# Performance work log

Hardware: AMD Instinct MI355X
Metric: run time of the kernel (lower is better)

The kernel has to match this reference:

```python
import jax, jax.numpy as jnp
import numpy as np

NEG_INF = -1.0e9  # matches torch masked_fill value (unused: no mask)

def setup_inputs() -> dict:
    key = jax.random.key(0)
    kq, kk, kv = jax.random.split(key, 3)
    B, Sq, Sk, D = 8, 2048, 2048, 512
    return {
        "query": jax.random.normal(kq, (B, Sq, D), dtype=jnp.float32),
        "key": jax.random.normal(kk, (B, Sk, D), dtype=jnp.float32),
        "value": jax.random.normal(kv, (B, Sk, D), dtype=jnp.float32),
        "temperature": jnp.ones((), dtype=jnp.float32),
    }

def reference(query, key, value, temperature):
    # Squared Euclidean distance via GEMM identity: ||q||^2 + ||k||^2 - 2 q.k
    # (same math as the broadcast sum((q-k)^2, -1), but without [B,Sq,Sk,D] tensor)
    q_sq = jnp.sum(query * query, axis=-1, keepdims=True)          # [B,Sq,1]
    k_sq = jnp.sum(key * key, axis=-1)[:, None, :]                 # [B,1,Sk]
    qk = jnp.einsum("bqd,bkd->bqk", query, key)                    # [B,Sq,Sk]
    distance_squared = q_sq + k_sq - 2.0 * qk
    similarity = -distance_squared / temperature
    attention_weights = jax.nn.softmax(similarity, axis=-1)        # [B,Sq,Sk]
    attended_values = jnp.einsum("bqk,bkd->bqd", attention_weights, value)
    return attended_values, attention_weights
```

## Files before the change

kernel.cpp:

```cpp
#include <hip/hip_runtime.h>

typedef __bf16 bf16_t;
typedef __bf16 bf16x8 __attribute__((ext_vector_type(8)));
typedef __bf16 bf16x4 __attribute__((ext_vector_type(4)));
typedef __bf16 bf16x2 __attribute__((ext_vector_type(2)));
typedef float f32x4 __attribute__((ext_vector_type(4)));

#define NB 8
#define SQ 2048
#define SK 2048
#define DD 512

#define BM 128
#define BN 128
#define BK 32
#define LDK 40
#define NBLK (SK / BN)

__global__ __launch_bounds__(256, 2) void logits_kernel(
    const float* __restrict__ Q, const float* __restrict__ K,
    const float* __restrict__ tempP, float* __restrict__ logits,
    float* __restrict__ Mpart, float* __restrict__ Spart) {
  __shared__ bf16_t qh[BM][LDK], ql[BM][LDK], kh[BN][LDK], kl[BN][LDK];
  __shared__ float ksred[BN][8];
  __shared__ float mred[BM][2], sred[BM][2];
  const int b = blockIdx.z;
  const int m0 = blockIdx.y * BM;
  const int n0 = blockIdx.x * BN;
  const int tid = threadIdx.x;
  const int lane = tid & 63;
  const int wave = tid >> 6;
  const int wm = (wave >> 1) * 64;
  const int wn = (wave & 1) * 64;
  const int lrow = lane & 15;
  const int quad = lane >> 4;

  const float* Qb = Q + (size_t)b * SQ * DD;
  const float* Kb = K + (size_t)b * SK * DD;

  const int srow = tid >> 3;
  const int scol = (tid & 7) * 4;

  const float* qbase = Qb + (size_t)(m0 + srow) * DD + scol;
  const float* kbase = Kb + (size_t)(n0 + srow) * DD + scol;

  f32x4 acc[4][4];
#pragma unroll
  for (int i = 0; i < 4; i++)
#pragma unroll
    for (int j = 0; j < 4; j++) acc[i][j] = (f32x4){0.f, 0.f, 0.f, 0.f};

  float kss[4] = {0.f, 0.f, 0.f, 0.f};

  float4 pq[4], pk[4];
#pragma unroll
  for (int i = 0; i < 4; i++) {
    pq[i] = *(const float4*)(qbase + (size_t)i * 32 * DD);
    pk[i] = *(const float4*)(kbase + (size_t)i * 32 * DD);
  }

  for (int k0 = 0; k0 < DD; k0 += BK) {
    __syncthreads();
#pragma unroll
    for (int i = 0; i < 4; i++) {
      const int r = srow + i * 32;
      float4 qv = pq[i], kv = pk[i];
      bf16_t q0 = (bf16_t)qv.x, q1 = (bf16_t)qv.y, q2 = (bf16_t)qv.z, q3 = (bf16_t)qv.w;
      bf16x4 qhv = {q0, q1, q2, q3};
      bf16x4 qlv = {(bf16_t)(qv.x - (float)q0), (bf16_t)(qv.y - (float)q1),
                    (bf16_t)(qv.z - (float)q2), (bf16_t)(qv.w - (float)q3)};
      bf16_t c0 = (bf16_t)kv.x, c1 = (bf16_t)kv.y, c2 = (bf16_t)kv.z, c3 = (bf16_t)kv.w;
      bf16x4 khv = {c0, c1, c2, c3};
      bf16x4 klv = {(bf16_t)(kv.x - (float)c0), (bf16_t)(kv.y - (float)c1),
                    (bf16_t)(kv.z - (float)c2), (bf16_t)(kv.w - (float)c3)};
      *(bf16x4*)&qh[r][scol] = qhv;
      *(bf16x4*)&ql[r][scol] = qlv;
      *(bf16x4*)&kh[r][scol] = khv;
      *(bf16x4*)&kl[r][scol] = klv;
      kss[i] = fmaf(kv.x, kv.x, kss[i]);
      kss[i] = fmaf(kv.y, kv.y, kss[i]);
      kss[i] = fmaf(kv.z, kv.z, kss[i]);
      kss[i] = fmaf(kv.w, kv.w, kss[i]);
    }
    __syncthreads();

    if (k0 + BK < DD) {
#pragma unroll
      for (int i = 0; i < 4; i++) {
        pq[i] = *(const float4*)(qbase + (size_t)i * 32 * DD + (k0 + BK));
        pk[i] = *(const float4*)(kbase + (size_t)i * 32 * DD + (k0 + BK));
      }
    }

    bf16x8 bh[4], bl[4];
#pragma unroll
    for (int ni = 0; ni < 4; ni++) {
      bh[ni] = *(const bf16x8*)&kh[wn + ni * 16 + lrow][quad * 8];
      bl[ni] = *(const bf16x8*)&kl[wn + ni * 16 + lrow][quad * 8];
    }
#pragma unroll
    for (int mi = 0; mi < 4; mi++) {
      bf16x8 ah = *(const bf16x8*)&qh[wm + mi * 16 + lrow][quad * 8];
      bf16x8 al = *(const bf16x8*)&ql[wm + mi * 16 + lrow][quad * 8];
#pragma unroll
      for (int ni = 0; ni < 4; ni++) {
        acc[mi][ni] = __builtin_amdgcn_mfma_f32_16x16x32_bf16(ah, bh[ni], acc[mi][ni], 0, 0, 0);
        acc[mi][ni] = __builtin_amdgcn_mfma_f32_16x16x32_bf16(ah, bl[ni], acc[mi][ni], 0, 0, 0);
        acc[mi][ni] = __builtin_amdgcn_mfma_f32_16x16x32_bf16(al, bh[ni], acc[mi][ni], 0, 0, 0);
      }
    }
  }

#pragma unroll
  for (int i = 0; i < 4; i++) ksred[srow + i * 32][tid & 7] = kss[i];
  __syncthreads();

  const float invT = 1.0f / tempP[0];
  float* Lb = logits + (size_t)b * SQ * SK;
  float ks4[4];
#pragma unroll
  for (int ni = 0; ni < 4; ni++) {
    const float* kr = ksred[wn + ni * 16 + lrow];
    ks4[ni] = ((kr[0] + kr[1]) + (kr[2] + kr[3])) +
              ((kr[4] + kr[5]) + (kr[6] + kr[7]));
  }

#pragma unroll
  for (int mi = 0; mi < 4; mi++) {
#pragma unroll
    for (int r = 0; r < 4; r++) {
      const int row = wm + mi * 16 + quad * 4 + r;
      float sv[4];
#pragma unroll
      for (int ni = 0; ni < 4; ni++) {
        sv[ni] = (2.0f * acc[mi][ni][r] - ks4[ni]) * invT;
        Lb[(size_t)(m0 + row) * SK + (n0 + wn + ni * 16 + lrow)] = sv[ni];
      }
      float rm = fmaxf(fmaxf(sv[0], sv[1]), fmaxf(sv[2], sv[3]));
      rm = fmaxf(rm, __shfl_xor(rm, 1));
      rm = fmaxf(rm, __shfl_xor(rm, 2));
      rm = fmaxf(rm, __shfl_xor(rm, 4));
      rm = fmaxf(rm, __shfl_xor(rm, 8));
      float rs = __expf(sv[0] - rm) + __expf(sv[1] - rm) +
                 __expf(sv[2] - rm) + __expf(sv[3] - rm);
      rs += __shfl_xor(rs, 1);
      rs += __shfl_xor(rs, 2);
      rs += __shfl_xor(rs, 4);
      rs += __shfl_xor(rs, 8);
      if (lrow == 0) {
        mred[row][wave & 1] = rm;
        sred[row][wave & 1] = rs;
      }
    }
  }
  __syncthreads();
  if (tid < BM) {
    const float ma = mred[tid][0], mb = mred[tid][1];
    const float M = fmaxf(ma, mb);
    const float S = sred[tid][0] * __expf(ma - M) + sred[tid][1] * __expf(mb - M);
    const size_t o = ((size_t)b * NBLK + blockIdx.x) * SQ + (m0 + tid);
    Mpart[o] = M;
    Spart[o] = S;
  }
}

__global__ __launch_bounds__(256) void vt_kernel(const float* __restrict__ V,
                                                 bf16_t* __restrict__ Vt) {
  const int b = blockIdx.y;
  const int k0 = blockIdx.x * 32;
  const int tid = threadIdx.x;
  const int p = tid & 15;
  const int c = tid >> 4;
  const float* Vb = V + (size_t)b * SK * DD;
  bf16_t* Vtb = Vt + (size_t)b * DD * SK;
  const int k = k0 + 2 * p;
#pragma unroll
  for (int j = 0; j < 8; j++) {
    const int d0 = 4 * c + 64 * j;
    float4 v0 = *(const float4*)(Vb + (size_t)k * DD + d0);
    float4 v1 = *(const float4*)(Vb + (size_t)(k + 1) * DD + d0);
    bf16x2 t0 = {(bf16_t)v0.x, (bf16_t)v1.x};
    bf16x2 t1 = {(bf16_t)v0.y, (bf16_t)v1.y};
    bf16x2 t2 = {(bf16_t)v0.z, (bf16_t)v1.z};
    bf16x2 t3 = {(bf16_t)v0.w, (bf16_t)v1.w};
    *(bf16x2*)(Vtb + (size_t)(d0 + 0) * SK + k) = t0;
    *(bf16x2*)(Vtb + (size_t)(d0 + 1) * SK + k) = t1;
    *(bf16x2*)(Vtb + (size_t)(d0 + 2) * SK + k) = t2;
    *(bf16x2*)(Vtb + (size_t)(d0 + 3) * SK + k) = t3;
  }
}

#define PM 64

__global__ __launch_bounds__(512, 2) void pv_kernel(
    float* __restrict__ L,
    const bf16_t* __restrict__ Vt,
    const float* __restrict__ Mpart, const float* __restrict__ Spart,
    float* __restrict__ O) {
  __shared__ float Msh[PM], Ssh[PM];
  const int bid = blockIdx.x;
  const int b = bid & 7;
  const int m0 = (bid >> 3) * PM;
  const int tid = threadIdx.x;
  const int lane = tid & 63;
  const int wave = tid >> 6;
  const int wn = wave * 64;
  const int lrow = lane & 15;
  const int quad = lane >> 4;

  float* Lb = L + (size_t)b * SQ * SK;
  const bf16_t* Vtb = Vt + (size_t)b * DD * SK;

  if (tid < 4 * PM) {
    const int row = tid >> 2;
    const int i0 = (tid & 3) * 4;
    float pm[4], ps[4];
#pragma unroll
    for (int j = 0; j < 4; j++) {
      const size_t o = ((size_t)b * NBLK + (i0 + j)) * SQ + (m0 + row);
      pm[j] = Mpart[o];
      ps[j] = Spart[o];
    }
    float m = fmaxf(fmaxf(pm[0], pm[1]), fmaxf(pm[2], pm[3]));
    m = fmaxf(m, __shfl_xor(m, 1));
    m = fmaxf(m, __shfl_xor(m, 2));
    float s = ps[0] * __expf(pm[0] - m) + ps[1] * __expf(pm[1] - m) +
              ps[2] * __expf(pm[2] - m) + ps[3] * __expf(pm[3] - m);
    s += __shfl_xor(s, 1);
    s += __shfl_xor(s, 2);
    if ((tid & 3) == 0) {
      Msh[row] = m;
      Ssh[row] = 1.0f / s;
    }
  }
  __syncthreads();

  float Mv[4], Sv[4];
  float* Arow[4];
  const bf16_t* Brow[4];
#pragma unroll
  for (int i = 0; i < 4; i++) {
    const int r = i * 16 + lrow;
    Mv[i] = Msh[r];
    Sv[i] = Ssh[r];
    Arow[i] = Lb + (size_t)(m0 + r) * SK + quad * 8;
    Brow[i] = Vtb + (size_t)(wn + r) * SK + quad * 8;
  }

  f32x4 acc[4][4];
#pragma unroll
  for (int i = 0; i < 4; i++)
#pragma unroll
    for (int j = 0; j < 4; j++) acc[i][j] = (f32x4){0.f, 0.f, 0.f, 0.f};

  float4 rawA[4][2], rawB[4][2];
  bf16x8 bb[4];

#pragma unroll
  for (int mi = 0; mi < 4; mi++) {
    rawA[mi][0] = *(const float4*)(Arow[mi]);
    rawA[mi][1] = *(const float4*)(Arow[mi] + 4);
    rawB[mi][0] = *(const float4*)(Arow[mi] + BK);
    rawB[mi][1] = *(const float4*)(Arow[mi] + BK + 4);
  }
#pragma unroll
  for (int ni = 0; ni < 4; ni++) bb[ni] = *(const bf16x8*)(Brow[ni]);

  auto process = [&](float4 (&buf)[4][2], const int kw) {
    float4 nw[4][2];
    bf16x8 af[4];
#pragma unroll
    for (int mi = 0; mi < 4; mi++) {
      float4 r0 = buf[mi][0], r1 = buf[mi][1];
      float e0 = __expf(r0.x - Mv[mi]) * Sv[mi];
      float e1 = __expf(r0.y - Mv[mi]) * Sv[mi];
      float e2 = __expf(r0.z - Mv[mi]) * Sv[mi];
      float e3 = __expf(r0.w - Mv[mi]) * Sv[mi];
      float e4 = __expf(r1.x - Mv[mi]) * Sv[mi];
      float e5 = __expf(r1.y - Mv[mi]) * Sv[mi];
      float e6 = __expf(r1.z - Mv[mi]) * Sv[mi];
      float e7 = __expf(r1.w - Mv[mi]) * Sv[mi];
      nw[mi][0] = make_float4(e0, e1, e2, e3);
      nw[mi][1] = make_float4(e4, e5, e6, e7);
      af[mi] = (bf16x8){(bf16_t)e0, (bf16_t)e1, (bf16_t)e2, (bf16_t)e3,
                        (bf16_t)e4, (bf16_t)e5, (bf16_t)e6, (bf16_t)e7};
    }
    if (kw + 2 * BK < SK) {
#pragma unroll
      for (int mi = 0; mi < 4; mi++) {
        buf[mi][0] = *(const float4*)(Arow[mi] + kw + 2 * BK);
        buf[mi][1] = *(const float4*)(Arow[mi] + kw + 2 * BK + 4);
      }
    }
#pragma unroll
    for (int mi = 0; mi < 4; mi++)
#pragma unroll
      for (int ni = 0; ni < 4; ni++)
        acc[mi][ni] = __builtin_amdgcn_mfma_f32_16x16x32_bf16(af[mi], bb[ni],
                                                              acc[mi][ni], 0, 0, 0);
    if (kw + BK < SK) {
#pragma unroll
      for (int ni = 0; ni < 4; ni++)
        bb[ni] = *(const bf16x8*)(Brow[ni] + kw + BK);
    }
    asm volatile("s_barrier" ::: "memory");
    if (wave == 0) {
#pragma unroll
      for (int mi = 0; mi < 4; mi++) {
        *(float4*)(Arow[mi] + kw) = nw[mi][0];
        *(float4*)(Arow[mi] + kw + 4) = nw[mi][1];
      }
    }
  };

  for (int k0 = 0; k0 < SK; k0 += 2 * BK) {
    process(rawA, k0);
    process(rawB, k0 + BK);
  }

  float* Ob = O + (size_t)b * SQ * DD;
#pragma unroll
  for (int ni = 0; ni < 4; ni++) {
    const int d = wn + ni * 16 + lrow;
#pragma unroll
    for (int mi = 0; mi < 4; mi++) {
      const int mbase = m0 + mi * 16 + quad * 4;
#pragma unroll
      for (int r = 0; r < 4; r++) {
        Ob[(size_t)(mbase + r) * DD + d] = acc[mi][ni][r];
      }
    }
  }
}

extern "C" void kernel_launch(void* const* d_in, const int* in_sizes, int n_in,
                              void* d_out, int out_size, void* d_ws, size_t ws_size,
                              hipStream_t stream) {
  const float* Q = (const float*)d_in[0];
  const float* K = (const float*)d_in[1];
  const float* V = (const float*)d_in[2];
  const float* T = (const float*)d_in[3];

  float* outv = (float*)d_out;
  float* logits = outv + (size_t)NB * SQ * DD;

  float* Mpart = (float*)d_ws;
  float* Spart = Mpart + (size_t)NB * NBLK * SQ;
  bf16_t* Vt = (bf16_t*)(Spart + (size_t)NB * NBLK * SQ);

  vt_kernel<<<dim3(SK / 32, NB), 256, 0, stream>>>(V, Vt);
  logits_kernel<<<dim3(SK / BN, SQ / BM, NB), 256, 0, stream>>>(Q, K, T, logits,
                                                                Mpart, Spart);
  pv_kernel<<<dim3(NB * (SQ / PM)), 512, 0, stream>>>(logits, Vt, Mpart, Spart, outv);
}
```

Measured before the change: 509.0 us.

## Stage normalized softmax rows in swizzled LDS before the PV MFMA loop

```diff
diff --git a/kernel.cpp b/kernel.cpp
--- a/kernel.cpp
+++ b/kernel.cpp
@@ -190,132 +190,124 @@
   }
 }
 
-#define PM 64
-
-__global__ __launch_bounds__(512, 2) void pv_kernel(
+#define PM 32
+
+__device__ __forceinline__ unsigned lds_addr(int row, unsigned kb) {
+  return (unsigned)row * 4096u + (kb ^ (unsigned)((row & 7) << 4));
+}
+
+__global__ __launch_bounds__(512, 1) void pv_kernel(
     float* __restrict__ L,
     const bf16_t* __restrict__ Vt,
     const float* __restrict__ Mpart, const float* __restrict__ Spart,
     float* __restrict__ O) {
+  __shared__ __align__(16) unsigned char wlds[PM * 4096];
   __shared__ float Msh[PM], Ssh[PM];
   const int bid = blockIdx.x;
   const int b = bid & 7;
   const int m0 = (bid >> 3) * PM;
   const int tid = threadIdx.x;
+
+  float* Lb = L + (size_t)b * SQ * SK;
+  const bf16_t* Vtb = Vt + (size_t)b * DD * SK;
+
+  {
+    const int row = tid >> 4;
+    const int j = tid & 15;
+    const size_t o = ((size_t)b * NBLK + j) * SQ + (m0 + row);
+    const float pm = Mpart[o];
+    const float ps = Spart[o];
+    float m = pm;
+    m = fmaxf(m, __shfl_xor(m, 1));
+    m = fmaxf(m, __shfl_xor(m, 2));
+    m = fmaxf(m, __shfl_xor(m, 4));
+    m = fmaxf(m, __shfl_xor(m, 8));
+    float s = ps * __expf(pm - m);
+    s += __shfl_xor(s, 1);
+    s += __shfl_xor(s, 2);
+    s += __shfl_xor(s, 4);
+    s += __shfl_xor(s, 8);
+    if (j == 0) {
+      Msh[row] = m;
+      Ssh[row] = 1.0f / s;
+    }
+  }
+  __syncthreads();
+
+  {
+    const int row = tid >> 4;
+    const int g = tid & 15;
+    float* lp = Lb + (size_t)(m0 + row) * SK;
+    const float M = Msh[row];
+    const float invS = Ssh[row];
+#pragma unroll 8
+    for (int j = 0; j < 32; j++) {
+      const int k = g * 4 + j * 64;
+      float4 v = *(const float4*)(lp + k);
+      const float w0 = __expf(v.x - M) * invS;
+      const float w1 = __expf(v.y - M) * invS;
+      const float w2 = __expf(v.z - M) * invS;
+      const float w3 = __expf(v.w - M) * invS;
+      *(float4*)(lp + k) = make_float4(w0, w1, w2, w3);
+      bf16x4 w4 = {(bf16_t)w0, (bf16_t)w1, (bf16_t)w2, (bf16_t)w3};
+      *(bf16x4*)(wlds + lds_addr(row, (unsigned)(k * 2))) = w4;
+    }
+  }
+  __syncthreads();
+
   const int lane = tid & 63;
   const int wave = tid >> 6;
   const int wn = wave * 64;
   const int lrow = lane & 15;
   const int quad = lane >> 4;
 
-  float* Lb = L + (size_t)b * SQ * SK;
-  const bf16_t* Vtb = Vt + (size_t)b * DD * SK;
-
-  if (tid < 4 * PM) {
-    const int row = tid >> 2;
-    const int i0 = (tid & 3) * 4;
-    float pm[4], ps[4];
-#pragma unroll
-    for (int j = 0; j < 4; j++) {
-      const size_t o = ((size_t)b * NBLK + (i0 + j)) * SQ + (m0 + row);
-      pm[j] = Mpart[o];
-      ps[j] = Spart[o];
-    }
-    float m = fmaxf(fmaxf(pm[0], pm[1]), fmaxf(pm[2], pm[3]));
-    m = fmaxf(m, __shfl_xor(m, 1));
-    m = fmaxf(m, __shfl_xor(m, 2));
-    float s = ps[0] * __expf(pm[0] - m) + ps[1] * __expf(pm[1] - m) +
-              ps[2] * __expf(pm[2] - m) + ps[3] * __expf(pm[3] - m);
-    s += __shfl_xor(s, 1);
-    s += __shfl_xor(s, 2);
-    if ((tid & 3) == 0) {
-      Msh[row] = m;
-      Ssh[row] = 1.0f / s;
-    }
-  }
-  __syncthreads();
-
-  float Mv[4], Sv[4];
-  float* Arow[4];
   const bf16_t* Brow[4];
 #pragma unroll
-  for (int i = 0; i < 4; i++) {
-    const int r = i * 16 + lrow;
-    Mv[i] = Msh[r];
-    Sv[i] = Ssh[r];
-    Arow[i] = Lb + (size_t)(m0 + r) * SK + quad * 8;
-    Brow[i] = Vtb + (size_t)(wn + r) * SK + quad * 8;
-  }
-
-  f32x4 acc[4][4];
-#pragma unroll
-  for (int i = 0; i < 4; i++)
+  for (int ni = 0; ni < 4; ni++)
+    Brow[ni] = Vtb + (size_t)(wn + ni * 16 + lrow) * SK + quad * 8;
+
+  f32x4 acc[2][4];
+#pragma unroll
+  for (int i = 0; i < 2; i++)
 #pragma unroll
     for (int j = 0; j < 4; j++) acc[i][j] = (f32x4){0.f, 0.f, 0.f, 0.f};
 
-  float4 rawA[4][2], rawB[4][2];
-  bf16x8 bb[4];
-
-#pragma unroll
-  for (int mi = 0; mi < 4; mi++) {
-    rawA[mi][0] = *(const float4*)(Arow[mi]);
-    rawA[mi][1] = *(const float4*)(Arow[mi] + 4);
-    rawB[mi][0] = *(const float4*)(Arow[mi] + BK);
-    rawB[mi][1] = *(const float4*)(Arow[mi] + BK + 4);
-  }
-#pragma unroll
-  for (int ni = 0; ni < 4; ni++) bb[ni] = *(const bf16x8*)(Brow[ni]);
-
-  auto process = [&](float4 (&buf)[4][2], const int kw) {
-    float4 nw[4][2];
-    bf16x8 af[4];
-#pragma unroll
-    for (int mi = 0; mi < 4; mi++) {
-      float4 r0 = buf[mi][0], r1 = buf[mi][1];
-      float e0 = __expf(r0.x - Mv[mi]) * Sv[mi];
-      float e1 = __expf(r0.y - Mv[mi]) * Sv[mi];
-      float e2 = __expf(r0.z - Mv[mi]) * Sv[mi];
-      float e3 = __expf(r0.w - Mv[mi]) * Sv[mi];
-      float e4 = __expf(r1.x - Mv[mi]) * Sv[mi];
-      float e5 = __expf(r1.y - Mv[mi]) * Sv[mi];
-      float e6 = __expf(r1.z - Mv[mi]) * Sv[mi];
-      float e7 = __expf(r1.w - Mv[mi]) * Sv[mi];
-      nw[mi][0] = make_float4(e0, e1, e2, e3);
-      nw[mi][1] = make_float4(e4, e5, e6, e7);
-      af[mi] = (bf16x8){(bf16_t)e0, (bf16_t)e1, (bf16_t)e2, (bf16_t)e3,
-                        (bf16_t)e4, (bf16_t)e5, (bf16_t)e6, (bf16_t)e7};
-    }
-    if (kw + 2 * BK < SK) {
-#pragma unroll
-      for (int mi = 0; mi < 4; mi++) {
-        buf[mi][0] = *(const float4*)(Arow[mi] + kw + 2 * BK);
-        buf[mi][1] = *(const float4*)(Arow[mi] + kw + 2 * BK + 4);
-      }
-    }
-#pragma unroll
-    for (int mi = 0; mi < 4; mi++)
+  bf16x8 b0[4], b1[4];
+#pragma unroll
+  for (int ni = 0; ni < 4; ni++) b0[ni] = *(const bf16x8*)(Brow[ni]);
+#pragma unroll
+  for (int ni = 0; ni < 4; ni++) b1[ni] = *(const bf16x8*)(Brow[ni] + BK);
+
+  for (int k0 = 0; k0 < SK; k0 += 2 * BK) {
+    bf16x8 a0[2], a1[2];
+#pragma unroll
+    for (int mi = 0; mi < 2; mi++) {
+      const int row = mi * 16 + lrow;
+      a0[mi] = *(const bf16x8*)(wlds + lds_addr(row, (unsigned)((k0 + quad * 8) * 2)));
+      a1[mi] = *(const bf16x8*)(wlds + lds_addr(row, (unsigned)((k0 + BK + quad * 8) * 2)));
+    }
+#pragma unroll
+    for (int mi = 0; mi < 2; mi++)
 #pragma unroll
       for (int ni = 0; ni < 4; ni++)
-        acc[mi][ni] = __builtin_amdgcn_mfma_f32_16x16x32_bf16(af[mi], bb[ni],
+        acc[mi][ni] = __builtin_amdgcn_mfma_f32_16x16x32_bf16(a0[mi], b0[ni],
                                                               acc[mi][ni], 0, 0, 0);
-    if (kw + BK < SK) {
+    if (k0 + 2 * BK < SK) {
 #pragma unroll
       for (int ni = 0; ni < 4; ni++)
-        bb[ni] = *(const bf16x8*)(Brow[ni] + kw + BK);
-    }
-    asm volatile("s_barrier" ::: "memory");
-    if (wave == 0) {
-#pragma unroll
-      for (int mi = 0; mi < 4; mi++) {
-        *(float4*)(Arow[mi] + kw) = nw[mi][0];
-        *(float4*)(Arow[mi] + kw + 4) = nw[mi][1];
-      }
-    }
-  };
-
-  for (int k0 = 0; k0 < SK; k0 += 2 * BK) {
-    process(rawA, k0);
-    process(rawB, k0 + BK);
+        b0[ni] = *(const bf16x8*)(Brow[ni] + k0 + 2 * BK);
+    }
+#pragma unroll
+    for (int mi = 0; mi < 2; mi++)
+#pragma unroll
+      for (int ni = 0; ni < 4; ni++)
+        acc[mi][ni] = __builtin_amdgcn_mfma_f32_16x16x32_bf16(a1[mi], b1[ni],
+                                                              acc[mi][ni], 0, 0, 0);
+    if (k0 + 3 * BK < SK) {
+#pragma unroll
+      for (int ni = 0; ni < 4; ni++)
+        b1[ni] = *(const bf16x8*)(Brow[ni] + k0 + 3 * BK);
+    }
   }
 
   float* Ob = O + (size_t)b * SQ * DD;
@@ -323,7 +315,7 @@
   for (int ni = 0; ni < 4; ni++) {
     const int d = wn + ni * 16 + lrow;
 #pragma unroll
-    for (int mi = 0; mi < 4; mi++) {
+    for (int mi = 0; mi < 2; mi++) {
       const int mbase = m0 + mi * 16 + quad * 4;
 #pragma unroll
       for (int r = 0; r < 4; r++) {
```

After: 474.5 us. -6.8%, faster.
